# Kernel optimization log

Measured on AMD Instinct MI355X. Metric: run time of the kernel, lower is better.

## Reference

```python
import jax, jax.numpy as jnp
import numpy as np

N_NODES = 100000
N_EDGES = 1600000
D_IN = 128
D_HID = 128


def setup_inputs() -> dict:
    key = jax.random.key(0)
    ks = jax.random.split(key, 8)
    s_in = 1.0 / np.sqrt(D_IN)
    s_h = 1.0 / np.sqrt(D_HID)
    return {
        "x": jax.random.normal(ks[0], (N_NODES, D_IN), dtype=jnp.float32),
        "edge_index": jax.random.randint(ks[1], (2, N_EDGES), 0, N_NODES, dtype=jnp.int32),
        "edge_weight": jax.random.uniform(ks[2], (N_EDGES,), dtype=jnp.float32),
        "W0l": jax.random.normal(ks[3], (D_IN, D_HID), dtype=jnp.float32) * s_in,
        "b0l": jnp.zeros((D_HID,), dtype=jnp.float32),
        "W0r": jax.random.normal(ks[4], (D_IN, D_HID), dtype=jnp.float32) * s_in,
        "W2l": jax.random.normal(ks[5], (D_HID, D_HID), dtype=jnp.float32) * s_h,
        "b2l": jnp.zeros((D_HID,), dtype=jnp.float32),
        "W2r": jax.random.normal(ks[6], (D_HID, D_HID), dtype=jnp.float32) * s_h,
    }


def _sage_conv(x, src, dst, Wl, bl, Wr):
    # PyG SAGEConv: mean-aggregate source features onto targets, then
    # out = lin_l(aggr) + lin_r(x)   (bias only on lin_l)
    msgs = x[src]  # [E, D] gather
    summed = jax.ops.segment_sum(msgs, dst, num_segments=N_NODES)  # [N, D]
    deg = jax.ops.segment_sum(jnp.ones((src.shape[0],), x.dtype), dst,
                              num_segments=N_NODES)
    mean = summed / jnp.maximum(deg, 1.0)[:, None]
    return mean @ Wl + bl + x @ Wr


def reference(x, edge_index, edge_weight, W0l, b0l, W0r, W2l, b2l, W2r):
    src, dst = edge_index[0], edge_index[1]
    # layer 0 (the only layer hit by `for i in range(num_layers-2)`)
    h = jax.nn.relu(_sage_conv(x, src, dst, W0l, b0l, W0r))
    mid_node_feats = [h]
    # layer num_layers-1 (layer 1 is constructed but never called in forward)
    fea = jax.nn.relu(_sage_conv(h, src, dst, W2l, b2l, W2r))
    # dropout is identity at inference (training=False)
    return (fea, *mid_node_feats)
```

## Files before the change

kernel.cpp:

```cpp
#include <hip/hip_runtime.h>
#include <hip/hip_bf16.h>

#define N_NODES 100000
#define N_EDGES 1600000
#define D 128
#define NF (N_NODES * D)

#define NGROUPS 8
#define NODES_PER_GROUP ((N_NODES + NGROUPS - 1) / NGROUPS)
#define EPB 4096

static __device__ __forceinline__ unsigned short f32_to_bf16_rne(float f) {
    unsigned u = __float_as_uint(f);
    unsigned lsb = (u >> 16) & 1u;
    u += 0x7fffu + lsb;
    return (unsigned short)(u >> 16);
}

__global__ __launch_bounds__(256) void convert_bf16_kernel(
    const float* __restrict__ in, unsigned* __restrict__ out, int n8) {
    int i = blockIdx.x * blockDim.x + threadIdx.x;
    if (i >= n8) return;
    const float4* p = (const float4*)(in + (size_t)i * 8);
    float4 a = p[0], b = p[1];
    uint4 o;
    o.x = (unsigned)f32_to_bf16_rne(a.x) | ((unsigned)f32_to_bf16_rne(a.y) << 16);
    o.y = (unsigned)f32_to_bf16_rne(a.z) | ((unsigned)f32_to_bf16_rne(a.w) << 16);
    o.z = (unsigned)f32_to_bf16_rne(b.x) | ((unsigned)f32_to_bf16_rne(b.y) << 16);
    o.w = (unsigned)f32_to_bf16_rne(b.z) | ((unsigned)f32_to_bf16_rne(b.w) << 16);
    ((uint4*)out)[i] = o;
}

__global__ __launch_bounds__(256) void deg_count_part_kernel(
    const int* __restrict__ dst, int* __restrict__ deg, int nE) {
    const int g = blockIdx.x & (NGROUPS - 1);
    const int chunk = blockIdx.x >> 3;
    const int base = chunk * EPB;
    const unsigned lo = (unsigned)(g * NODES_PER_GROUP);
    for (int i = threadIdx.x; i < EPB; i += 256) {
        int e = base + i;
        if (e >= nE) break;
        int d = dst[e];
        if ((unsigned)(d - lo) < (unsigned)NODES_PER_GROUP) {
            atomicAdd(&deg[d], 1);
        }
    }
}

__global__ __launch_bounds__(1024) void scan1_kernel(
    const int* __restrict__ deg, int* __restrict__ rowptr,
    int* __restrict__ bsums, int n) {
    __shared__ int buf[1024];
    int i = blockIdx.x * 1024 + threadIdx.x;
    int v = (i < n) ? deg[i] : 0;
    buf[threadIdx.x] = v;
    __syncthreads();
    for (int off = 1; off < 1024; off <<= 1) {
        int t = (threadIdx.x >= off) ? buf[threadIdx.x - off] : 0;
        __syncthreads();
        if (threadIdx.x >= off) buf[threadIdx.x] += t;
        __syncthreads();
    }
    if (i < n) rowptr[i] = buf[threadIdx.x] - v;
    if (threadIdx.x == 1023) bsums[blockIdx.x] = buf[1023];
}

__global__ __launch_bounds__(128) void scan2_kernel(int* __restrict__ bsums,
                                                    int nb) {
    __shared__ int buf[128];
    int v = (threadIdx.x < nb) ? bsums[threadIdx.x] : 0;
    buf[threadIdx.x] = v;
    __syncthreads();
    for (int off = 1; off < 128; off <<= 1) {
        int t = (threadIdx.x >= off) ? buf[threadIdx.x - off] : 0;
        __syncthreads();
        if (threadIdx.x >= off) buf[threadIdx.x] += t;
        __syncthreads();
    }
    if (threadIdx.x < nb) bsums[threadIdx.x] = buf[threadIdx.x] - v;
}

__global__ __launch_bounds__(1024) void scan3_kernel(
    int* __restrict__ rowptr, const int* __restrict__ bsums,
    int* __restrict__ cursor, int n, int nE) {
    int i = blockIdx.x * 1024 + threadIdx.x;
    if (i < n) {
        int r = rowptr[i] + bsums[blockIdx.x];
        rowptr[i] = r;
        cursor[i] = r;
    }
    if (i == 0) rowptr[n] = nE;
}

__global__ __launch_bounds__(256) void csr_fill_part_kernel(
    const int* __restrict__ src,
    const int* __restrict__ dst,
    int* __restrict__ cursor,
    int* __restrict__ col, int nE) {
    const int g = blockIdx.x & (NGROUPS - 1);
    const int chunk = blockIdx.x >> 3;
    const int base = chunk * EPB;
    const unsigned lo = (unsigned)(g * NODES_PER_GROUP);
    for (int i = threadIdx.x; i < EPB; i += 256) {
        int e = base + i;
        if (e >= nE) break;
        int d = dst[e];
        if ((unsigned)(d - lo) < (unsigned)NODES_PER_GROUP) {
            int p = atomicAdd(&cursor[d], 1);
            col[p] = src[e];
        }
    }
}

__global__ __launch_bounds__(256) void aggregate_mean_bf16_kernel(
    const unsigned short* __restrict__ Xb,
    const int* __restrict__ rowptr,
    const int* __restrict__ col,
    float* __restrict__ mean) {
    int node = (int)((blockIdx.x * blockDim.x + threadIdx.x) >> 6);
    int lane = threadIdx.x & 63;
    if (node >= N_NODES) return;
    int beg = rowptr[node];
    int end = rowptr[node + 1];
    float a0x = 0.f, a0y = 0.f, a1x = 0.f, a1y = 0.f;
    int p = beg;
    for (; p + 3 < end; p += 4) {
        int s0 = col[p];
        int s1 = col[p + 1];
        int s2 = col[p + 2];
        int s3 = col[p + 3];
        unsigned v0 = ((const unsigned*)(Xb + (size_t)s0 * D))[lane];
        unsigned v1 = ((const unsigned*)(Xb + (size_t)s1 * D))[lane];
        unsigned v2 = ((const unsigned*)(Xb + (size_t)s2 * D))[lane];
        unsigned v3 = ((const unsigned*)(Xb + (size_t)s3 * D))[lane];
        a0x += __uint_as_float(v0 << 16) + __uint_as_float(v1 << 16);
        a0y += __uint_as_float(v0 & 0xffff0000u) + __uint_as_float(v1 & 0xffff0000u);
        a1x += __uint_as_float(v2 << 16) + __uint_as_float(v3 << 16);
        a1y += __uint_as_float(v2 & 0xffff0000u) + __uint_as_float(v3 & 0xffff0000u);
    }
    for (; p < end; ++p) {
        int s = col[p];
        unsigned v = ((const unsigned*)(Xb + (size_t)s * D))[lane];
        a0x += __uint_as_float(v << 16);
        a0y += __uint_as_float(v & 0xffff0000u);
    }
    int dg = end - beg;
    float invd = 1.0f / (float)(dg > 1 ? dg : 1);
    float2 o;
    o.x = (a0x + a1x) * invd;
    o.y = (a0y + a1y) * invd;
    ((float2*)(mean + (size_t)node * D))[lane] = o;
}

__global__ __launch_bounds__(256) void aggregate_mean_kernel(
    const float* __restrict__ X,
    const int* __restrict__ rowptr,
    const int* __restrict__ col,
    float* __restrict__ mean) {
    int node = (int)((blockIdx.x * blockDim.x + threadIdx.x) >> 6);
    int lane = threadIdx.x & 63;
    if (node >= N_NODES) return;
    int beg = rowptr[node];
    int end = rowptr[node + 1];
    float a0x = 0.f, a0y = 0.f, a1x = 0.f, a1y = 0.f;
    int p = beg;
    for (; p + 3 < end; p += 4) {
        int s0 = col[p];
        int s1 = col[p + 1];
        int s2 = col[p + 2];
        int s3 = col[p + 3];
        float2 v0 = ((const float2*)(X + (size_t)s0 * D))[lane];
        float2 v1 = ((const float2*)(X + (size_t)s1 * D))[lane];
        float2 v2 = ((const float2*)(X + (size_t)s2 * D))[lane];
        float2 v3 = ((const float2*)(X + (size_t)s3 * D))[lane];
        a0x += v0.x + v1.x;
        a0y += v0.y + v1.y;
        a1x += v2.x + v3.x;
        a1y += v2.y + v3.y;
    }
    for (; p < end; ++p) {
        int s = col[p];
        float2 v = ((const float2*)(X + (size_t)s * D))[lane];
        a0x += v.x;
        a0y += v.y;
    }
    int dg = end - beg;
    float invd = 1.0f / (float)(dg > 1 ? dg : 1);
    float2 o;
    o.x = (a0x + a1x) * invd;
    o.y = (a0y + a1y) * invd;
    ((float2*)(mean + (size_t)node * D))[lane] = o;
}

#define BM 128
#define BK 32

__global__ __launch_bounds__(256) void sage_gemm_kernel(
    const float* __restrict__ Amean,
    const float* __restrict__ Aself,
    const float* __restrict__ Wl,
    const float* __restrict__ Wr,
    const float* __restrict__ bias,
    float* __restrict__ Out,
    unsigned short* __restrict__ OutBf,
    int nrows) {
    __shared__ float As[BM][BK + 4];
    __shared__ float Bs[BK][132];

    const int tid = threadIdx.x;
    const int row0 = blockIdx.x * BM;
    const int tx = tid & 15;
    const int ty = tid >> 4;

    float acc[8][8];
#pragma unroll
    for (int i = 0; i < 8; i++)
#pragma unroll
        for (int j = 0; j < 8; j++) acc[i][j] = 0.f;

    for (int step = 0; step < 8; ++step) {
        const int k0 = step * BK;
        const float* A = (k0 < 128) ? Amean : Aself;
        const float* W = (k0 < 128) ? Wl : Wr;
        const int kc = k0 & 127;

        {
            int r = tid >> 1;
            int kk0 = (tid & 1) * 16;
            int gr = row0 + r;
            if (gr >= nrows) gr = nrows - 1;
            const float4* srcp = (const float4*)(A + (size_t)gr * D + kc + kk0);
#pragma unroll
            for (int q = 0; q < 4; q++) {
                float4 v = srcp[q];
                *(float4*)&As[r][kk0 + 4 * q] = v;
            }
        }
        {
            int kk = tid >> 3;
            int c = tid & 7;
            const float4* srcp = (const float4*)(W + (size_t)(kc + kk) * D);
#pragma unroll
            for (int q = 0; q < 4; q++) {
                float4 v = srcp[c + 8 * q];
                *(float4*)&Bs[kk][(c + 8 * q) * 4] = v;
            }
        }
        __syncthreads();

#pragma unroll
        for (int kk = 0; kk < BK; ++kk) {
            float a[8], b[8];
#pragma unroll
            for (int i = 0; i < 8; i++) a[i] = As[ty * 8 + i][kk];
            float4 b0 = *(const float4*)&Bs[kk][tx * 4];
            float4 b1 = *(const float4*)&Bs[kk][64 + tx * 4];
            b[0] = b0.x; b[1] = b0.y; b[2] = b0.z; b[3] = b0.w;
            b[4] = b1.x; b[5] = b1.y; b[6] = b1.z; b[7] = b1.w;
#pragma unroll
            for (int i = 0; i < 8; i++)
#pragma unroll
                for (int j = 0; j < 8; j++) acc[i][j] += a[i] * b[j];
        }
        __syncthreads();
    }

    float4 bv0 = *(const float4*)&bias[tx * 4];
    float4 bv1 = *(const float4*)&bias[64 + tx * 4];
#pragma unroll
    for (int i = 0; i < 8; i++) {
        int gr = row0 + ty * 8 + i;
        if (gr < nrows) {
            float4 o0, o1;
            o0.x = fmaxf(acc[i][0] + bv0.x, 0.f);
            o0.y = fmaxf(acc[i][1] + bv0.y, 0.f);
            o0.z = fmaxf(acc[i][2] + bv0.z, 0.f);
            o0.w = fmaxf(acc[i][3] + bv0.w, 0.f);
            o1.x = fmaxf(acc[i][4] + bv1.x, 0.f);
            o1.y = fmaxf(acc[i][5] + bv1.y, 0.f);
            o1.z = fmaxf(acc[i][6] + bv1.z, 0.f);
            o1.w = fmaxf(acc[i][7] + bv1.w, 0.f);
            *(float4*)(Out + (size_t)gr * D + tx * 4) = o0;
            *(float4*)(Out + (size_t)gr * D + 64 + tx * 4) = o1;
            if (OutBf) {
                uint2 p0, p1;
                p0.x = (unsigned)f32_to_bf16_rne(o0.x) |
                       ((unsigned)f32_to_bf16_rne(o0.y) << 16);
                p0.y = (unsigned)f32_to_bf16_rne(o0.z) |
                       ((unsigned)f32_to_bf16_rne(o0.w) << 16);
                p1.x = (unsigned)f32_to_bf16_rne(o1.x) |
                       ((unsigned)f32_to_bf16_rne(o1.y) << 16);
                p1.y = (unsigned)f32_to_bf16_rne(o1.z) |
                       ((unsigned)f32_to_bf16_rne(o1.w) << 16);
                *(uint2*)(OutBf + (size_t)gr * D + tx * 4) = p0;
                *(uint2*)(OutBf + (size_t)gr * D + 64 + tx * 4) = p1;
            }
        }
    }
}

extern "C" void kernel_launch(void* const* d_in, const int* in_sizes, int n_in,
                              void* d_out, int out_size, void* d_ws,
                              size_t ws_size, hipStream_t stream) {
    const float* x   = (const float*)d_in[0];
    const int*   ei  = (const int*)d_in[1];
    const float* W0l = (const float*)d_in[3];
    const float* b0l = (const float*)d_in[4];
    const float* W0r = (const float*)d_in[5];
    const float* W2l = (const float*)d_in[6];
    const float* b2l = (const float*)d_in[7];
    const float* W2r = (const float*)d_in[8];

    const int* src = ei;
    const int* dst = ei + N_EDGES;

    float* fea = (float*)d_out;
    float* h   = (float*)d_out + NF;
    float* meanbuf = fea;

    char* ws = (char*)d_ws;
    int* deg    = (int*)ws;
    int* rowptr = (int*)(ws + 400000);
    int* bsums  = (int*)(ws + 800032);
    int* cursor = (int*)(ws + 800544);
    int* col    = (int*)(ws + 1200544);
    unsigned short* xb = (unsigned short*)(ws + 7600640);
    const bool use_bf16 = (ws_size >= (size_t)33200640);

    const int nScanBlocks = (N_NODES + 1023) / 1024;
    const int nChunks = (N_EDGES + EPB - 1) / EPB;

    hipMemsetAsync(deg, 0, N_NODES * sizeof(int), stream);
    deg_count_part_kernel<<<nChunks * NGROUPS, 256, 0, stream>>>(dst, deg,
                                                                 N_EDGES);
    scan1_kernel<<<nScanBlocks, 1024, 0, stream>>>(deg, rowptr, bsums, N_NODES);
    scan2_kernel<<<1, 128, 0, stream>>>(bsums, nScanBlocks);
    scan3_kernel<<<nScanBlocks, 1024, 0, stream>>>(rowptr, bsums, cursor,
                                                   N_NODES, N_EDGES);
    csr_fill_part_kernel<<<nChunks * NGROUPS, 256, 0, stream>>>(src, dst,
                                                                cursor, col,
                                                                N_EDGES);

    const int aggGrid = (N_NODES * 64 + 255) / 256;
    const int gemmGrid = (N_NODES + BM - 1) / BM;

    if (use_bf16) {
        convert_bf16_kernel<<<(NF / 8 + 255) / 256, 256, 0, stream>>>(
            x, (unsigned*)xb, NF / 8);

        aggregate_mean_bf16_kernel<<<aggGrid, 256, 0, stream>>>(xb, rowptr,
                                                                col, meanbuf);
        sage_gemm_kernel<<<gemmGrid, 256, 0, stream>>>(meanbuf, x, W0l, W0r,
                                                       b0l, h, xb, N_NODES);

        aggregate_mean_bf16_kernel<<<aggGrid, 256, 0, stream>>>(xb, rowptr,
                                                                col, meanbuf);
        sage_gemm_kernel<<<gemmGrid, 256, 0, stream>>>(meanbuf, h, W2l, W2r,
                                                       b2l, fea, (unsigned short*)nullptr,
                                                       N_NODES);
    } else {
        aggregate_mean_kernel<<<aggGrid, 256, 0, stream>>>(x, rowptr, col,
                                                           meanbuf);
        sage_gemm_kernel<<<gemmGrid, 256, 0, stream>>>(meanbuf, x, W0l, W0r,
                                                       b0l, h, (unsigned short*)nullptr,
                                                       N_NODES);
        aggregate_mean_kernel<<<aggGrid, 256, 0, stream>>>(h, rowptr, col,
                                                           meanbuf);
        sage_gemm_kernel<<<gemmGrid, 256, 0, stream>>>(meanbuf, h, W2l, W2r,
                                                       b2l, fea, (unsigned short*)nullptr,
                                                       N_NODES);
    }
}
```

Before: 644.6 us.

## Halve GEMM row tile and transpose A tile in shared memory

The SAGE GEMM row tile drops from 128 to 64 rows, so each thread holds a 4x8 accumulator block instead of 8x8. The A tile is now stored transposed in LDS, which lets each thread read its four A values with one float4 load instead of eight scalar loads. This lowers register pressure and doubles the number of blocks, which should raise occupancy for the 100k-row GEMM. In exchange, each loaded B tile is reused across fewer rows, and the transposed scalar stores into LDS may cause bank conflicts. The host launch grid must use the new BM; the hidden code presumably derives it from the macro.

```diff
diff --git a/kernel.cpp b/kernel.cpp
--- a/kernel.cpp
+++ b/kernel.cpp
@@ -192,7 +192,7 @@
     ((float2*)(mean + (size_t)node * D))[lane] = o;
 }
 
-#define BM 128
+#define BM 64
 #define BK 32
 
 __global__ __launch_bounds__(256) void sage_gemm_kernel(
@@ -204,7 +204,7 @@
     float* __restrict__ Out,
     unsigned short* __restrict__ OutBf,
     int nrows) {
-    __shared__ float As[BM][BK + 4];
+    __shared__ float AsT[BK][68];
     __shared__ float Bs[BK][132];
 
     const int tid = threadIdx.x;
@@ -212,29 +212,29 @@
     const int tx = tid & 15;
     const int ty = tid >> 4;
 
-    float acc[8][8];
-#pragma unroll
-    for (int i = 0; i < 8; i++)
+    float acc[4][8];
+#pragma unroll
+    for (int i = 0; i < 4; i++)
 #pragma unroll
         for (int j = 0; j < 8; j++) acc[i][j] = 0.f;
 
     for (int step = 0; step < 8; ++step) {
-        const int k0 = step * BK;
-        const float* A = (k0 < 128) ? Amean : Aself;
-        const float* W = (k0 < 128) ? Wl : Wr;
-        const int kc = k0 & 127;
+        const float* A = (step < 4) ? Amean : Aself;
+        const float* W = (step < 4) ? Wl : Wr;
+        const int kc = (step & 3) * BK;
 
         {
-            int r = tid >> 1;
-            int kk0 = (tid & 1) * 16;
+            int r = tid & 63;
+            int kb = tid >> 6;
             int gr = row0 + r;
             if (gr >= nrows) gr = nrows - 1;
-            const float4* srcp = (const float4*)(A + (size_t)gr * D + kc + kk0);
-#pragma unroll
-            for (int q = 0; q < 4; q++) {
-                float4 v = srcp[q];
-                *(float4*)&As[r][kk0 + 4 * q] = v;
-            }
+            const float4* srcp = (const float4*)(A + (size_t)gr * D + kc + kb * 8);
+            float4 v0 = srcp[0], v1 = srcp[1];
+            int k0 = kb * 8;
+            AsT[k0 + 0][r] = v0.x; AsT[k0 + 1][r] = v0.y;
+            AsT[k0 + 2][r] = v0.z; AsT[k0 + 3][r] = v0.w;
+            AsT[k0 + 4][r] = v1.x; AsT[k0 + 5][r] = v1.y;
+            AsT[k0 + 6][r] = v1.z; AsT[k0 + 7][r] = v1.w;
         }
         {
             int kk = tid >> 3;
@@ -250,15 +250,13 @@
 
 #pragma unroll
         for (int kk = 0; kk < BK; ++kk) {
-            float a[8], b[8];
-#pragma unroll
-            for (int i = 0; i < 8; i++) a[i] = As[ty * 8 + i][kk];
+            float4 av = *(const float4*)&AsT[kk][ty * 4];
             float4 b0 = *(const float4*)&Bs[kk][tx * 4];
             float4 b1 = *(const float4*)&Bs[kk][64 + tx * 4];
-            b[0] = b0.x; b[1] = b0.y; b[2] = b0.z; b[3] = b0.w;
-            b[4] = b1.x; b[5] = b1.y; b[6] = b1.z; b[7] = b1.w;
-#pragma unroll
-            for (int i = 0; i < 8; i++)
+            float a[4] = {av.x, av.y, av.z, av.w};
+            float b[8] = {b0.x, b0.y, b0.z, b0.w, b1.x, b1.y, b1.z, b1.w};
+#pragma unroll
+            for (int i = 0; i < 4; i++)
 #pragma unroll
                 for (int j = 0; j < 8; j++) acc[i][j] += a[i] * b[j];
         }
@@ -268,8 +266,8 @@
     float4 bv0 = *(const float4*)&bias[tx * 4];
     float4 bv1 = *(const float4*)&bias[64 + tx * 4];
 #pragma unroll
-    for (int i = 0; i < 8; i++) {
-        int gr = row0 + ty * 8 + i;
+    for (int i = 0; i < 4; i++) {
+        int gr = row0 + ty * 4 + i;
         if (gr < nrows) {
             float4 o0, o1;
             o0.x = fmaxf(acc[i][0] + bv0.x, 0.f);
```

Result: faster. 627.5 us (-2.7%).
